# Performance work log

Hardware: AMD Instinct MI355X
Metric: run time of the kernel (lower is better)

Reference implementation:

```python
import jax, jax.numpy as jnp
import numpy as np

N = 50000   # nodes
E = 800000  # edges (avg degree 16)
D = 128     # input feature size
H = 256     # hidden size
P = 512     # pool_size
O = 64      # output size


def setup_inputs() -> dict:
    key = jax.random.key(0)
    ks = jax.random.split(key, 9)
    x = jax.random.normal(ks[0], (N, D), dtype=jnp.float32)
    src = jax.random.randint(ks[1], (E,), 0, N)
    dst = jax.random.randint(ks[2], (E,), 0, N)
    w = lambda k, sh: jax.random.normal(k, sh, dtype=jnp.float32) * 0.05
    return {
        "x": x, "src": src, "dst": dst,
        "aggW0": w(ks[3], (D, P)),      # aggregator W1, layer 0
        "aggW1": w(ks[4], (H, P)),
        "aggW2": w(ks[5], (H, P)),
        "linW0": w(ks[6], (D + P, H)),  # linear after concat, layer 0
        "linW1": w(ks[7], (H + P, H)),
        "linW2": w(ks[8], (H + P, O)),
    }


def _sage_layer(x, src, dst, aggW, linW, activate):
    # DGLMaxPoolAggregator: project sources, scatter-max to destinations
    h = x @ aggW                                   # [N, P]
    hN = jax.ops.segment_max(h[src], dst, num_segments=x.shape[0])  # [N, P]
    # DGL fills zeros for nodes with no in-edges; segment_max gives -inf
    hN = jnp.where(jnp.isneginf(hN), jnp.zeros_like(hN), hN)
    out = jnp.concatenate([x, hN], axis=1) @ linW  # [N, out]
    return jax.nn.relu(out) if activate else out


def reference(x, src, dst, aggW0, aggW1, aggW2, linW0, linW1, linW2):
    x = _sage_layer(x, src, dst, aggW0, linW0, True)   # layer 0 (+relu, dropout p=0)
    x = _sage_layer(x, src, dst, aggW1, linW1, True)   # layer 1 (+relu)
    return _sage_layer(x, src, dst, aggW2, linW2, False)  # output layer
```

## Files before the change

### kernel.cpp

```cpp
#include <hip/hip_runtime.h>
#include <hip/hip_bf16.h>

#define MN 50000
#define NE 800000
#define DD 128
#define HH 256
#define PP 512
#define OO 64

typedef unsigned short bf16r;
using short8 = __attribute__((ext_vector_type(8))) short;
using ushort8 = __attribute__((ext_vector_type(8))) unsigned short;
using f32x4 = __attribute__((ext_vector_type(4))) float;

__device__ __forceinline__ float b2f(bf16r s) {
  unsigned int u = ((unsigned int)s) << 16;
  float f;
  __builtin_memcpy(&f, &u, 4);
  return f;
}
__device__ __forceinline__ bf16r f2b(float f) {
  unsigned int u;
  __builtin_memcpy(&u, &f, 4);
  u += 0x7fffu + ((u >> 16) & 1u);
  return (bf16r)(u >> 16);
}
__device__ __forceinline__ unsigned short keymap(unsigned short u) {
  return u ^ ((u & 0x8000u) ? 0x7FFFu : 0u);
}
__device__ __forceinline__ void stC(float* p, float v) { *p = v; }
__device__ __forceinline__ void stC(bf16r* p, float v) { *p = f2b(v); }

__device__ __forceinline__ void async16(void* lds, const void* g) {
  auto l = reinterpret_cast<__attribute__((address_space(3))) char*>(
      reinterpret_cast<uintptr_t>(lds));
  auto gp = reinterpret_cast<const __attribute__((address_space(1))) char*>(
      reinterpret_cast<uintptr_t>(g));
  __builtin_amdgcn_global_load_lds(gp, l, 16, 0, 0);
}

__global__ void zero_ints(int* __restrict__ p, int n) {
  int i = blockIdx.x * blockDim.x + threadIdx.x;
  if (i < n) p[i] = 0;
}

__global__ void conv_bf16(const float* __restrict__ in, bf16r* __restrict__ out, int n4) {
  int i = blockIdx.x * 256 + threadIdx.x;
  if (i < n4) {
    float4 v = reinterpret_cast<const float4*>(in)[i];
    ushort4 u;
    u.x = f2b(v.x); u.y = f2b(v.y); u.z = f2b(v.z); u.w = f2b(v.w);
    reinterpret_cast<ushort4*>(out)[i] = u;
  }
}

__device__ __forceinline__ void tw1(const float* B, bf16r* BT, int i, int K, int Nc) {
  int k = i / Nc, n = i - k * Nc;
  BT[(size_t)n * K + k] = f2b(B[i]);
}
__global__ void transpose_all(const float* __restrict__ b0, const float* __restrict__ b1,
                              const float* __restrict__ b2, const float* __restrict__ b3,
                              const float* __restrict__ b4, const float* __restrict__ b5,
                              bf16r* __restrict__ t0, bf16r* __restrict__ t1,
                              bf16r* __restrict__ t2, bf16r* __restrict__ t3,
                              bf16r* __restrict__ t4, bf16r* __restrict__ t5) {
  int idx = blockIdx.x * 256 + threadIdx.x;
  if (idx < 196608) {
    if (idx < 65536) tw1(b0, t0, idx, 128, 512);
    else tw1(b1, t1, idx - 65536, 256, 512);
  } else if (idx < 491520) {
    if (idx < 327680) tw1(b2, t2, idx - 196608, 256, 512);
    else tw1(b3, t3, idx - 327680, 640, 256);
  } else if (idx < 737280) {
    if (idx < 688128) tw1(b4, t4, idx - 491520, 768, 256);
    else tw1(b5, t5, idx - 688128, 768, 64);
  }
}

__global__ void count_edges(const int* __restrict__ dst, int* __restrict__ counts) {
  int e = blockIdx.x * blockDim.x + threadIdx.x;
  if (e < NE) atomicAdd(&counts[dst[e]], 1);
}

__global__ __launch_bounds__(1024) void scan_local(const int* __restrict__ counts,
                                                   int* __restrict__ row_ptr,
                                                   int* __restrict__ bsum) {
  __shared__ int buf[1024];
  const int b = blockIdx.x, t = threadIdx.x;
  int2 c2 = reinterpret_cast<const int2*>(counts)[b * 1024 + t];
  int tsum = c2.x + c2.y;
  buf[t] = tsum;
  __syncthreads();
  int s = tsum;
  for (int off = 1; off < 1024; off <<= 1) {
    int add = (t >= off) ? buf[t - off] : 0;
    __syncthreads();
    s += add;
    buf[t] = s;
    __syncthreads();
  }
  int excl = s - tsum;
  int2 o;
  o.x = excl;
  o.y = excl + c2.x;
  reinterpret_cast<int2*>(row_ptr)[b * 1024 + t] = o;
  if (t == 1023) bsum[b] = s;
}

__global__ __launch_bounds__(1024) void scan_add(int* __restrict__ row_ptr,
                                                 int* __restrict__ cursor,
                                                 const int* __restrict__ bsum) {
  const int b = blockIdx.x, t = threadIdx.x;
  int off = 0;
  for (int j = 0; j < b; ++j) off += bsum[j];
  int i0 = b * 2048 + 2 * t;
#pragma unroll
  for (int k = 0; k < 2; ++k) {
    int i = i0 + k;
    if (i <= MN) {
      int v = row_ptr[i] + off;
      row_ptr[i] = v;
      if (i < MN) cursor[i] = v;
    }
  }
}

__global__ void scatter_edges(const int* __restrict__ src, const int* __restrict__ dst,
                              int* __restrict__ cursor, int* __restrict__ esrc) {
  int e = blockIdx.x * blockDim.x + threadIdx.x;
  if (e < NE) {
    int d = dst[e];
    int pos = atomicAdd(&cursor[d], 1);
    esrc[pos] = src[e];
  }
}

__global__ __launch_bounds__(256) void seg_max(const bf16r* __restrict__ h,
                                               const int* __restrict__ row_ptr,
                                               const int* __restrict__ esrc,
                                               bf16r* __restrict__ hN) {
  const int node = blockIdx.x * 4 + (threadIdx.x >> 6);
  if (node >= MN) return;
  const int lane = threadIdx.x & 63;
  const int g = lane >> 4;
  const int sl = lane & 15;
  const int colbase = blockIdx.y * 128 + sl * 8;
  const int beg = row_ptr[node];
  const int end = row_ptr[node + 1];
  short8 m8;
#pragma unroll
  for (int j = 0; j < 8; ++j) m8[j] = (short)0x807F;

  for (int cb = beg; cb < end; cb += 16) {
    int e0 = esrc[min(cb + g, end - 1)];
    int e1 = esrc[min(cb + 4 + g, end - 1)];
    int e2 = esrc[min(cb + 8 + g, end - 1)];
    int e3 = esrc[min(cb + 12 + g, end - 1)];
    short8 u0 = *reinterpret_cast<const short8*>(h + ((size_t)e0 << 9) + colbase);
    short8 u1 = *reinterpret_cast<const short8*>(h + ((size_t)e1 << 9) + colbase);
    short8 u2 = *reinterpret_cast<const short8*>(h + ((size_t)e2 << 9) + colbase);
    short8 u3 = *reinterpret_cast<const short8*>(h + ((size_t)e3 << 9) + colbase);
    m8 = __builtin_elementwise_max(m8, __builtin_elementwise_max(
        __builtin_elementwise_max(u0, u1), __builtin_elementwise_max(u2, u3)));
  }
#pragma unroll
  for (int mask = 16; mask <= 32; mask <<= 1) {
    int4 vi;
    __builtin_memcpy(&vi, &m8, 16);
    int4 ot;
    ot.x = __shfl_xor(vi.x, mask);
    ot.y = __shfl_xor(vi.y, mask);
    ot.z = __shfl_xor(vi.z, mask);
    ot.w = __shfl_xor(vi.w, mask);
    short8 o8;
    __builtin_memcpy(&o8, &ot, 16);
    m8 = __builtin_elementwise_max(m8, o8);
  }
  if (lane < 16) {
    ushort8 o;
    if (beg == end) {
#pragma unroll
      for (int j = 0; j < 8; ++j) o[j] = 0;
    } else {
#pragma unroll
      for (int j = 0; j < 8; ++j) o[j] = keymap((unsigned short)m8[j]);
    }
    *reinterpret_cast<ushort8*>(hN + (size_t)node * PP + colbase) = o;
  }
}

template <int T, int BM, int BN, int NCB, int WMC, int WNC, bool DUAL, bool RELU,
          bool KEYED, typename TO>
__global__ __launch_bounds__(T) void gemm_mfma(
    const bf16r* __restrict__ A1, int K1, const bf16r* __restrict__ A2, int K2,
    const bf16r* __restrict__ BT, int Ktot, TO* __restrict__ C, int M, int NC) {
  constexpr int BK = 32;
  constexpr int WM = BM / WMC;
  constexpr int WN = BN / WNC;
  constexpr int FM = WM / 16, FN = WN / 16;
  constexpr int ACH = (BM * 64) / (T * 16);
  constexpr int BCH = (BN * 64) / (T * 16);
  __shared__ short As[2][BM * BK];
  __shared__ short Bs[2][BN * BK];
  const int tid = threadIdx.x;
  const int lane = tid & 63;
  const int wv = tid >> 6;
  const int wr = wv / WNC, wc = wv % WNC;
  const int nwg = gridDim.x;
  const int q = nwg >> 3, r = nwg & 7;
  const int xcd = blockIdx.x & 7, slot = blockIdx.x >> 3;
  const int wgid = (xcd < r ? xcd * (q + 1) : r * (q + 1) + (xcd - r) * q) + slot;
  const int m0 = (wgid / NCB) * BM;
  const int n0 = (wgid % NCB) * BN;

  const int NT1 = K1 / BK;
  const int NT = NT1 + (DUAL ? K2 / BK : 0);

  auto stage = [&](int t, int b) {
    const int o = tid * 16;
#pragma unroll
    for (int c = 0; c < ACH; ++c) {
      int oo = o + c * (T * 16);
      int row = oo >> 6, colb = oo & 63;
      const char* g;
      if (!DUAL || t < NT1)
        g = (const char*)A1 + ((size_t)(m0 + row) * K1 + t * BK) * 2 + colb;
      else
        g = (const char*)A2 + ((size_t)(m0 + row) * K2 + (t - NT1) * BK) * 2 + colb;
      async16((char*)&As[b][0] + oo, g);
    }
#pragma unroll
    for (int c = 0; c < BCH; ++c) {
      int oo = o + c * (T * 16);
      int row = oo >> 6, colb = oo & 63;
      const char* g = (const char*)BT + ((size_t)(n0 + row) * Ktot + t * BK) * 2 + colb;
      async16((char*)&Bs[b][0] + oo, g);
    }
  };

  f32x4 acc[FM][FN];
#pragma unroll
  for (int i = 0; i < FM; ++i)
#pragma unroll
    for (int j = 0; j < FN; ++j)
#pragma unroll
      for (int r2 = 0; r2 < 4; ++r2) acc[i][j][r2] = 0.f;

  stage(0, 0);
  __syncthreads();
  for (int t = 0; t < NT; ++t) {
    const int b = t & 1;
    if (t + 1 < NT) stage(t + 1, b ^ 1);
    short8 af[FM], bfv[FN];
#pragma unroll
    for (int i = 0; i < FM; ++i)
      af[i] = *(const short8*)(&As[b][0] + (wr * WM + i * 16 + (lane & 15)) * BK +
                               (lane >> 4) * 8);
#pragma unroll
    for (int j = 0; j < FN; ++j)
      bfv[j] = *(const short8*)(&Bs[b][0] + (wc * WN + j * 16 + (lane & 15)) * BK +
                                (lane >> 4) * 8);
#pragma unroll
    for (int i = 0; i < FM; ++i)
#pragma unroll
      for (int j = 0; j < FN; ++j)
        acc[i][j] =
            __builtin_amdgcn_mfma_f32_16x16x32_bf16(af[i], bfv[j], acc[i][j], 0, 0, 0);
    __syncthreads();
  }

  const int crow0 = wr * WM + (lane >> 4) * 4;
  const int ccol0 = wc * WN + (lane & 15);
#pragma unroll
  for (int i = 0; i < FM; ++i)
#pragma unroll
    for (int j = 0; j < FN; ++j)
#pragma unroll
      for (int r2 = 0; r2 < 4; ++r2) {
        int row = m0 + crow0 + i * 16 + r2;
        if (row < M) {
          float v = acc[i][j][r2];
          if (RELU) v = fmaxf(v, 0.f);
          TO* p = &C[(size_t)row * NC + n0 + ccol0 + j * 16];
          if (KEYED) {
            *(bf16r*)p = keymap(f2b(v));
          } else {
            stC(p, v);
          }
        }
      }
}

extern "C" void kernel_launch(void* const* d_in, const int* in_sizes, int n_in,
                              void* d_out, int out_size, void* d_ws, size_t ws_size,
                              hipStream_t stream) {
  const float* x = (const float*)d_in[0];
  const int* src = (const int*)d_in[1];
  const int* dst = (const int*)d_in[2];
  const float* aggW0 = (const float*)d_in[3];
  const float* aggW1 = (const float*)d_in[4];
  const float* aggW2 = (const float*)d_in[5];
  const float* linW0 = (const float*)d_in[6];
  const float* linW1 = (const float*)d_in[7];
  const float* linW2 = (const float*)d_in[8];
  float* out = (float*)d_out;

  char* ws = (char*)d_ws;
  size_t off = 0;
  auto alloc = [&](size_t bytes) {
    void* p = ws + off;
    off = (off + bytes + 255) & ~(size_t)255;
    return p;
  };
  bf16r* h = (bf16r*)alloc((size_t)MN * PP * 2);
  bf16r* hN = (bf16r*)alloc((size_t)MN * PP * 2);
  bf16r* act1 = (bf16r*)alloc((size_t)MN * HH * 2);
  bf16r* act2 = (bf16r*)alloc((size_t)MN * HH * 2);
  bf16r* xb = (bf16r*)alloc((size_t)MN * DD * 2);
  bf16r* aggW0T = (bf16r*)alloc(512 * 128 * 2);
  bf16r* aggW1T = (bf16r*)alloc(512 * 256 * 2);
  bf16r* aggW2T = (bf16r*)alloc(512 * 256 * 2);
  bf16r* linW0T = (bf16r*)alloc(640 * 256 * 2);
  bf16r* linW1T = (bf16r*)alloc(768 * 256 * 2);
  bf16r* linW2T = (bf16r*)alloc(768 * 64 * 2);
  int* row_ptr = (int*)alloc(51264 * 4);
  int* cursor = (int*)alloc(MN * 4);
  int* counts = (int*)alloc(51264 * 4);
  int* bsum = (int*)alloc(32 * 4);
  int* esrc = (int*)alloc(NE * 4);

  zero_ints<<<(51264 + 255) / 256, 256, 0, stream>>>(counts, 51264);
  count_edges<<<(NE + 255) / 256, 256, 0, stream>>>(dst, counts);
  scan_local<<<25, 1024, 0, stream>>>(counts, row_ptr, bsum);
  scan_add<<<25, 1024, 0, stream>>>(row_ptr, cursor, bsum);
  scatter_edges<<<(NE + 255) / 256, 256, 0, stream>>>(src, dst, cursor, esrc);

  conv_bf16<<<((MN * DD / 4) + 255) / 256, 256, 0, stream>>>(x, xb, MN * DD / 4);
  transpose_all<<<(737280 + 255) / 256, 256, 0, stream>>>(
      aggW0, aggW1, aggW2, linW0, linW1, linW2,
      aggW0T, aggW1T, aggW2T, linW0T, linW1T, linW2T);

  const int RB256 = (MN + 255) / 256;
  const int RB128 = (MN + 127) / 128;
  dim3 gagg(RB256 * 4);
  dim3 glin(RB256 * 2);
  dim3 gout(RB128);
  dim3 gseg((MN + 3) / 4, 4);

  gemm_mfma<512, 256, 128, 4, 4, 2, false, false, true, bf16r><<<gagg, 512, 0, stream>>>(
      xb, DD, (const bf16r*)nullptr, 0, aggW0T, DD, h, MN, PP);
  seg_max<<<gseg, 256, 0, stream>>>(h, row_ptr, esrc, hN);
  gemm_mfma<512, 256, 128, 2, 4, 2, true, true, false, bf16r><<<glin, 512, 0, stream>>>(
      xb, DD, hN, PP, linW0T, DD + PP, act1, MN, HH);

  gemm_mfma<512, 256, 128, 4, 4, 2, false, false, true, bf16r><<<gagg, 512, 0, stream>>>(
      act1, HH, (const bf16r*)nullptr, 0, aggW1T, HH, h, MN, PP);
  seg_max<<<gseg, 256, 0, stream>>>(h, row_ptr, esrc, hN);
  gemm_mfma<512, 256, 128, 2, 4, 2, true, true, false, bf16r><<<glin, 512, 0, stream>>>(
      act1, HH, hN, PP, linW1T, HH + PP, act2, MN, HH);

  gemm_mfma<512, 256, 128, 4, 4, 2, false, false, true, bf16r><<<gagg, 512, 0, stream>>>(
      act2, HH, (const bf16r*)nullptr, 0, aggW2T, HH, h, MN, PP);
  seg_max<<<gseg, 256, 0, stream>>>(h, row_ptr, esrc, hN);
  gemm_mfma<256, 128, 64, 1, 4, 1, true, false, false, float><<<gout, 256, 0, stream>>>(
      act2, HH, hN, PP, linW2T, HH + PP, out, MN, OO);
}
```

Measured before the change: 613.6 us.

## Triple-buffer GEMM LDS stages with explicit vmcnt waits and compile-time K dims

The MFMA GEMM moves from a double-buffered loop with two __syncthreads per iteration to a three-stage LDS ring. It issues loads two tiles ahead and waits with explicit s_waitcnt vmcnt plus a single s_barrier per iteration. K sizes and output stride become template constants, so the K loop can be fully unrolled and address math folded. This is meant to hide global-load latency and cut barrier overhead, at the cost of more LDS per block, which may lower occupancy. The vmcnt literal only holds when each stage issues exactly three loads, and a static_assert enforces this.

```diff
diff --git a/kernel.cpp b/kernel.cpp
--- a/kernel.cpp
+++ b/kernel.cpp
@@ -189,19 +189,23 @@
   }
 }
 
-template <int T, int BM, int BN, int NCB, int WMC, int WNC, bool DUAL, bool RELU,
-          bool KEYED, typename TO>
+template <int T, int BM, int BN, int NCB, int WMC, int WNC, int K1T, int K2T,
+          int NCT, bool RELU, bool KEYED, typename TO>
 __global__ __launch_bounds__(T) void gemm_mfma(
-    const bf16r* __restrict__ A1, int K1, const bf16r* __restrict__ A2, int K2,
-    const bf16r* __restrict__ BT, int Ktot, TO* __restrict__ C, int M, int NC) {
+    const bf16r* __restrict__ A1, const bf16r* __restrict__ A2,
+    const bf16r* __restrict__ BT, TO* __restrict__ C, int M) {
   constexpr int BK = 32;
+  constexpr int Ktot = K1T + K2T;
+  constexpr int NT1 = K1T / BK;
+  constexpr int NT = Ktot / BK;
   constexpr int WM = BM / WMC;
   constexpr int WN = BN / WNC;
   constexpr int FM = WM / 16, FN = WN / 16;
   constexpr int ACH = (BM * 64) / (T * 16);
   constexpr int BCH = (BN * 64) / (T * 16);
-  __shared__ short As[2][BM * BK];
-  __shared__ short Bs[2][BN * BK];
+  static_assert(ACH + BCH == 3, "vmcnt(3) literal assumes 3 loads per stage");
+  __shared__ short As[3][BM * BK];
+  __shared__ short Bs[3][BN * BK];
   const int tid = threadIdx.x;
   const int lane = tid & 63;
   const int wv = tid >> 6;
@@ -213,9 +217,6 @@
   const int m0 = (wgid / NCB) * BM;
   const int n0 = (wgid % NCB) * BN;
 
-  const int NT1 = K1 / BK;
-  const int NT = NT1 + (DUAL ? K2 / BK : 0);
-
   auto stage = [&](int t, int b) {
     const int o = tid * 16;
 #pragma unroll
@@ -223,10 +224,10 @@
       int oo = o + c * (T * 16);
       int row = oo >> 6, colb = oo & 63;
       const char* g;
-      if (!DUAL || t < NT1)
-        g = (const char*)A1 + ((size_t)(m0 + row) * K1 + t * BK) * 2 + colb;
+      if (K2T == 0 || t < NT1)
+        g = (const char*)A1 + ((size_t)(m0 + row) * K1T + t * BK) * 2 + colb;
       else
-        g = (const char*)A2 + ((size_t)(m0 + row) * K2 + (t - NT1) * BK) * 2 + colb;
+        g = (const char*)A2 + ((size_t)(m0 + row) * K2T + (t - NT1) * BK) * 2 + colb;
       async16((char*)&As[b][0] + oo, g);
     }
 #pragma unroll
@@ -247,10 +248,15 @@
       for (int r2 = 0; r2 < 4; ++r2) acc[i][j][r2] = 0.f;
 
   stage(0, 0);
-  __syncthreads();
+  stage(1, 1);
+#pragma unroll
   for (int t = 0; t < NT; ++t) {
-    const int b = t & 1;
-    if (t + 1 < NT) stage(t + 1, b ^ 1);
+    if (t + 1 < NT)
+      asm volatile("s_waitcnt vmcnt(3)" ::: "memory");
+    else
+      asm volatile("s_waitcnt vmcnt(0)" ::: "memory");
+    __builtin_amdgcn_s_barrier();
+    const int b = t % 3;
     short8 af[FM], bfv[FN];
 #pragma unroll
     for (int i = 0; i < FM; ++i)
@@ -266,7 +272,7 @@
       for (int j = 0; j < FN; ++j)
         acc[i][j] =
             __builtin_amdgcn_mfma_f32_16x16x32_bf16(af[i], bfv[j], acc[i][j], 0, 0, 0);
-    __syncthreads();
+    if (t + 2 < NT) stage(t + 2, (t + 2) % 3);
   }
 
   const int crow0 = wr * WM + (lane >> 4) * 4;
@@ -281,7 +287,7 @@
         if (row < M) {
           float v = acc[i][j][r2];
           if (RELU) v = fmaxf(v, 0.f);
-          TO* p = &C[(size_t)row * NC + n0 + ccol0 + j * 16];
+          TO* p = &C[(size_t)row * NCT + n0 + ccol0 + j * 16];
           if (KEYED) {
             *(bf16r*)p = keymap(f2b(v));
           } else {
@@ -347,21 +353,21 @@
   dim3 gout(RB128);
   dim3 gseg((MN + 3) / 4, 4);
 
-  gemm_mfma<512, 256, 128, 4, 4, 2, false, false, true, bf16r><<<gagg, 512, 0, stream>>>(
-      xb, DD, (const bf16r*)nullptr, 0, aggW0T, DD, h, MN, PP);
+  gemm_mfma<512, 256, 128, 4, 4, 2, 128, 0, 512, false, true, bf16r>
+      <<<gagg, 512, 0, stream>>>(xb, (const bf16r*)nullptr, aggW0T, h, MN);
   seg_max<<<gseg, 256, 0, stream>>>(h, row_ptr, esrc, hN);
-  gemm_mfma<512, 256, 128, 2, 4, 2, true, true, false, bf16r><<<glin, 512, 0, stream>>>(
-      xb, DD, hN, PP, linW0T, DD + PP, act1, MN, HH);
-
-  gemm_mfma<512, 256, 128, 4, 4, 2, false, false, true, bf16r><<<gagg, 512, 0, stream>>>(
-      act1, HH, (const bf16r*)nullptr, 0, aggW1T, HH, h, MN, PP);
+  gemm_mfma<512, 256, 128, 2, 4, 2, 128, 512, 256, true, false, bf16r>
+      <<<glin, 512, 0, stream>>>(xb, hN, linW0T, act1, MN);
+
+  gemm_mfma<512, 256, 128, 4, 4, 2, 256, 0, 512, false, true, bf16r>
+      <<<gagg, 512, 0, stream>>>(act1, (const bf16r*)nullptr, aggW1T, h, MN);
   seg_max<<<gseg, 256, 0, stream>>>(h, row_ptr, esrc, hN);
-  gemm_mfma<512, 256, 128, 2, 4, 2, true, true, false, bf16r><<<glin, 512, 0, stream>>>(
-      act1, HH, hN, PP, linW1T, HH + PP, act2, MN, HH);
-
-  gemm_mfma<512, 256, 128, 4, 4, 2, false, false, true, bf16r><<<gagg, 512, 0, stream>>>(
-      act2, HH, (const bf16r*)nullptr, 0, aggW2T, HH, h, MN, PP);
+  gemm_mfma<512, 256, 128, 2, 4, 2, 256, 512, 256, true, false, bf16r>
+      <<<glin, 512, 0, stream>>>(act1, hN, linW1T, act2, MN);
+
+  gemm_mfma<512, 256, 128, 4, 4, 2, 256, 0, 512, false, true, bf16r>
+      <<<gagg, 512, 0, stream>>>(act2, (const bf16r*)nullptr, aggW2T, h, MN);
   seg_max<<<gseg, 256, 0, stream>>>(h, row_ptr, esrc, hN);
-  gemm_mfma<256, 128, 64, 1, 4, 1, true, false, false, float><<<gout, 256, 0, stream>>>(
-      act2, HH, hN, PP, linW2T, HH + PP, out, MN, OO);
-}
+  gemm_mfma<256, 128, 64, 1, 4, 1, 256, 512, 64, false, false, float>
+      <<<gout, 256, 0, stream>>>(act2, hN, linW2T, out, MN);
+}
```

Measured after the change: 607.3 us. Within noise of the previous version (-1.0%).
